# Performance work log

Measured on AMD Instinct MI355X. Metric: run time of the kernel, lower is better.

Reference implementation:

```python
import jax, jax.numpy as jnp
import numpy as np

N = 100000
E = 1600000
IN_C, HID_C, OUT_C = 128, 128, 64


def setup_inputs() -> dict:
    key = jax.random.key(0)
    k = jax.random.split(key, 8)
    x = jax.random.normal(k[0], (N, IN_C), dtype=jnp.float32)
    edge_index = jax.random.randint(k[1], (2, E), 0, N, dtype=jnp.int64)
    edge_attr = jax.random.uniform(k[2], (E,), dtype=jnp.float32)
    # Glorot-ish init for GCNConv weights, zero bias (PyG default)
    W1 = jax.random.normal(k[3], (IN_C, HID_C), dtype=jnp.float32) / np.sqrt(IN_C)
    b1 = jnp.zeros((HID_C,), dtype=jnp.float32)
    W2 = jax.random.normal(k[4], (HID_C, OUT_C), dtype=jnp.float32) / np.sqrt(HID_C)
    b2 = jnp.zeros((OUT_C,), dtype=jnp.float32)
    return {"x": x, "edge_index": edge_index, "edge_attr": edge_attr,
            "W1": W1, "b1": b1, "W2": W2, "b2": b2}


def _gcn_conv(x, W, b, src, dst, ew):
    """PyG GCNConv: add self-loops (weight 1), symmetric normalization,
    aggregate x@W over edges src->dst, add bias."""
    n = x.shape[0]
    loop = jnp.arange(n, dtype=src.dtype)
    src_f = jnp.concatenate([src, loop])            # [E+N]
    dst_f = jnp.concatenate([dst, loop])
    ew_f = jnp.concatenate([ew, jnp.ones((n,), dtype=ew.dtype)])
    deg = jax.ops.segment_sum(ew_f, dst_f, num_segments=n)  # [N]
    dis = jnp.where(deg > 0, jax.lax.rsqrt(jnp.maximum(deg, 1e-12)), 0.0)
    norm = dis[src_f] * ew_f * dis[dst_f]           # [E+N]
    h = x @ W                                       # [N, C_out]
    msg = norm[:, None] * h[src_f]                  # [E+N, C_out] gather
    out = jax.ops.segment_sum(msg, dst_f, num_segments=n)   # scatter-add
    return out + b


def reference(x, edge_index, edge_attr, W1, b1, W2, b2):
    src, dst = edge_index[0], edge_index[1]
    h = _gcn_conv(x, W1, b1, src, dst, edge_attr)
    h = jax.nn.relu(h)
    # dropout is identity in eval mode (training=False)
    out = _gcn_conv(h, W2, b2, src, dst, edge_attr)
    return out
```

## Files before the change

### kernel.cpp

```cpp
#include <hip/hip_runtime.h>

#define NN 100000
#define EE 1600000
#define NB 391

typedef unsigned int uint;
typedef unsigned short ushort;
typedef unsigned long long u64;

#define FIXMASK ((1ull << 40) - 1)

__device__ inline ushort f2bf(float f) {
    uint u = __float_as_uint(f);
    return (ushort)((u + 0x7fffu + ((u >> 16) & 1u)) >> 16);
}
__device__ inline float bf_lo(uint u) { return __uint_as_float(u << 16); }
__device__ inline float bf_hi(uint u) { return __uint_as_float(u & 0xffff0000u); }

__global__ void k_init(u64* __restrict__ dh) {
    int i = blockIdx.x * blockDim.x + threadIdx.x;
    if (i < NN) dh[i] = 0ull;
}

__global__ void k_dh(const int* __restrict__ dst, const float* __restrict__ ew,
                     u64* __restrict__ dh) {
    int e = blockIdx.x * blockDim.x + threadIdx.x;
    if (e >= EE) return;
    int d = dst[e];
    u64 w = (u64)(ew[e] * 16777216.0f + 0.5f);
    atomicAdd(&dh[d], (1ull << 40) | w);
}

__global__ __launch_bounds__(256) void k_scan_blk(const u64* __restrict__ dh,
                                                  float* __restrict__ dis,
                                                  int* __restrict__ rowptr,
                                                  int* __restrict__ bsum) {
    __shared__ int buf[2][256];
    int t = threadIdx.x;
    int i = blockIdx.x * 256 + t;
    int v = 0;
    if (i < NN) {
        u64 p = dh[i];
        v = (int)(p >> 40);
        float deg = 1.0f + (float)(p & FIXMASK) * (1.0f / 16777216.0f);
        dis[i] = rsqrtf(deg);
    }
    int pi = 0;
    buf[0][t] = v;
    __syncthreads();
    for (int off = 1; off < 256; off <<= 1) {
        int po = pi ^ 1;
        int add = (t >= off) ? buf[pi][t - off] : 0;
        buf[po][t] = buf[pi][t] + add;
        __syncthreads();
        pi = po;
    }
    int incl = buf[pi][t];
    if (i < NN) rowptr[i] = incl - v;
    if (t == 255) bsum[blockIdx.x] = incl;
}

__global__ __launch_bounds__(512) void k_scan_top(int* __restrict__ bsum) {
    __shared__ int buf[2][512];
    int t = threadIdx.x;
    int v = (t < NB) ? bsum[t] : 0;
    int pi = 0;
    buf[0][t] = v;
    __syncthreads();
    for (int off = 1; off < 512; off <<= 1) {
        int po = pi ^ 1;
        int add = (t >= off) ? buf[pi][t - off] : 0;
        buf[po][t] = buf[pi][t] + add;
        __syncthreads();
        pi = po;
    }
    int incl = buf[pi][t];
    if (t < NB) bsum[t] = incl - v;
}

__global__ void k_scan_add(int* __restrict__ rowptr, const int* __restrict__ bsum,
                           int* __restrict__ cursor) {
    int i = blockIdx.x * 256 + threadIdx.x;
    if (i < NN) {
        int r = rowptr[i] + bsum[i >> 8];
        rowptr[i] = r;
        cursor[i] = r;
    }
    if (i == 0) rowptr[NN] = EE;
}

__global__ void k_scatter(const int* __restrict__ src, const int* __restrict__ dst,
                          const float* __restrict__ ew, const float* __restrict__ dis,
                          int* __restrict__ cursor, int2* __restrict__ epk) {
    int e = blockIdx.x * blockDim.x + threadIdx.x;
    if (e >= EE) return;
    int d = dst[e];
    int s = src[e];
    int pos = atomicAdd(&cursor[d], 1);
    float w = dis[s] * ew[e];
    epk[pos] = make_int2(s, __float_as_int(w));
}

__global__ __launch_bounds__(256) void k_gemm1(const float* __restrict__ x,
                                               const float* __restrict__ W,
                                               ushort* __restrict__ h) {
    __shared__ float Wl[128 * 128];
    __shared__ float xt[128 * 32];
    int t = threadIdx.x;
    int rb = blockIdx.x * 32;

    const float4* W4 = (const float4*)W;
    float4* Wl4 = (float4*)Wl;
#pragma unroll
    for (int i = 0; i < 16; i++) Wl4[t + 256 * i] = W4[t + 256 * i];

#pragma unroll
    for (int i = 0; i < 4; i++) {
        int idx = t + 256 * i;
        int r = idx >> 5;
        int c4 = idx & 31;
        float4 v = ((const float4*)(x + (size_t)(rb + r) * 128))[c4];
        int kc = c4 << 2;
        xt[(kc + 0) * 32 + r] = v.x;
        xt[(kc + 1) * 32 + r] = v.y;
        xt[(kc + 2) * 32 + r] = v.z;
        xt[(kc + 3) * 32 + r] = v.w;
    }
    __syncthreads();

    int tc = t & 31;
    int tr = t >> 5;
    float acc[4][4] = {};
#pragma unroll 4
    for (int k = 0; k < 128; k++) {
        float4 wv = ((const float4*)(Wl + k * 128))[tc];
        float4 xv = ((const float4*)(xt + k * 32))[tr];
        float xs[4] = {xv.x, xv.y, xv.z, xv.w};
        float ws[4] = {wv.x, wv.y, wv.z, wv.w};
#pragma unroll
        for (int r = 0; r < 4; r++)
#pragma unroll
            for (int c = 0; c < 4; c++) acc[r][c] += xs[r] * ws[c];
    }
#pragma unroll
    for (int r = 0; r < 4; r++) {
        int row = rb + tr * 4 + r;
        ushort4 o = {f2bf(acc[r][0]), f2bf(acc[r][1]), f2bf(acc[r][2]), f2bf(acc[r][3])};
        ((ushort4*)(h + (size_t)row * 128))[tc] = o;
    }
}

__global__ __launch_bounds__(256) void k_gemm2(const float* __restrict__ a,
                                               const float* __restrict__ W,
                                               ushort* __restrict__ h) {
    __shared__ float Wl[128 * 64];
    __shared__ float at[128 * 64];
    int t = threadIdx.x;
    int rb = blockIdx.x * 64;

    const float4* W4 = (const float4*)W;
    float4* Wl4 = (float4*)Wl;
#pragma unroll
    for (int i = 0; i < 8; i++) Wl4[t + 256 * i] = W4[t + 256 * i];

#pragma unroll
    for (int i = 0; i < 8; i++) {
        int idx = t + 256 * i;
        int r = idx >> 5;
        int c4 = idx & 31;
        int row = rb + r;
        if (row >= NN) row = NN - 1;
        float4 v = ((const float4*)(a + (size_t)row * 128))[c4];
        int kc = c4 << 2;
        at[(kc + 0) * 64 + r] = v.x;
        at[(kc + 1) * 64 + r] = v.y;
        at[(kc + 2) * 64 + r] = v.z;
        at[(kc + 3) * 64 + r] = v.w;
    }
    __syncthreads();

    int tc = t & 15;
    int tr = t >> 4;
    float acc[4][4] = {};
#pragma unroll 4
    for (int k = 0; k < 128; k++) {
        float4 wv = ((const float4*)(Wl + k * 64))[tc];
        float4 av = ((const float4*)(at + k * 64))[tr];
        float as[4] = {av.x, av.y, av.z, av.w};
        float ws[4] = {wv.x, wv.y, wv.z, wv.w};
#pragma unroll
        for (int r = 0; r < 4; r++)
#pragma unroll
            for (int c = 0; c < 4; c++) acc[r][c] += as[r] * ws[c];
    }
#pragma unroll
    for (int r = 0; r < 4; r++) {
        int row = rb + tr * 4 + r;
        if (row < NN) {
            ushort4 o = {f2bf(acc[r][0]), f2bf(acc[r][1]), f2bf(acc[r][2]), f2bf(acc[r][3])};
            ((ushort4*)(h + (size_t)row * 64))[tc] = o;
        }
    }
}

__global__ __launch_bounds__(256) void k_agg1(const int* __restrict__ rowptr,
                                              const int2* __restrict__ epk,
                                              const float* __restrict__ dis,
                                              const ushort* __restrict__ h,
                                              const float* __restrict__ b,
                                              float* __restrict__ a) {
    int wid = (blockIdx.x * blockDim.x + threadIdx.x) >> 6;
    int lane = threadIdx.x & 63;
    if (wid >= NN) return;
    int beg = rowptr[wid], end = rowptr[wid + 1];
    const uint* hp = (const uint*)h;
    uint us = hp[(size_t)wid * 64 + lane];
    float di = dis[wid];
    float2 bv = ((const float2*)b)[lane];

    float2 acc0 = {0.f, 0.f}, acc1 = {0.f, 0.f};
    float2 acc2 = {0.f, 0.f}, acc3 = {0.f, 0.f};
    int j = beg;
    for (; j + 3 < end; j += 4) {
        int2 p0 = epk[j];
        int2 p1 = epk[j + 1];
        int2 p2 = epk[j + 2];
        int2 p3 = epk[j + 3];
        uint u0 = hp[(size_t)p0.x * 64 + lane];
        uint u1 = hp[(size_t)p1.x * 64 + lane];
        uint u2 = hp[(size_t)p2.x * 64 + lane];
        uint u3 = hp[(size_t)p3.x * 64 + lane];
        float w0 = __int_as_float(p0.y);
        float w1 = __int_as_float(p1.y);
        float w2 = __int_as_float(p2.y);
        float w3 = __int_as_float(p3.y);
        acc0.x += w0 * bf_lo(u0); acc0.y += w0 * bf_hi(u0);
        acc1.x += w1 * bf_lo(u1); acc1.y += w1 * bf_hi(u1);
        acc2.x += w2 * bf_lo(u2); acc2.y += w2 * bf_hi(u2);
        acc3.x += w3 * bf_lo(u3); acc3.y += w3 * bf_hi(u3);
    }
    for (; j < end; j++) {
        int2 p0 = epk[j];
        float w0 = __int_as_float(p0.y);
        uint u0 = hp[(size_t)p0.x * 64 + lane];
        acc0.x += w0 * bf_lo(u0); acc0.y += w0 * bf_hi(u0);
    }
    float sx = (acc0.x + acc1.x) + (acc2.x + acc3.x);
    float sy = (acc0.y + acc1.y) + (acc2.y + acc3.y);
    float ox = di * sx + di * di * bf_lo(us) + bv.x;
    float oy = di * sy + di * di * bf_hi(us) + bv.y;
    float2 o = {fmaxf(ox, 0.f), fmaxf(oy, 0.f)};
    ((float2*)a)[(size_t)wid * 64 + lane] = o;
}

__global__ __launch_bounds__(256) void k_agg2(const int* __restrict__ rowptr,
                                              const int2* __restrict__ epk,
                                              const float* __restrict__ dis,
                                              const ushort* __restrict__ h,
                                              const float* __restrict__ b,
                                              float* __restrict__ out) {
    int wid = (blockIdx.x * blockDim.x + threadIdx.x) >> 6;
    int lane = threadIdx.x & 63;
    if (wid >= NN) return;
    int beg = rowptr[wid], end = rowptr[wid + 1];
    float hv = __uint_as_float(((uint)h[(size_t)wid * 64 + lane]) << 16);
    float di = dis[wid];
    float bl = b[lane];

    float acc0 = 0.f, acc1 = 0.f, acc2 = 0.f, acc3 = 0.f;
    int j = beg;
    for (; j + 3 < end; j += 4) {
        int2 p0 = epk[j];
        int2 p1 = epk[j + 1];
        int2 p2 = epk[j + 2];
        int2 p3 = epk[j + 3];
        float v0 = __uint_as_float(((uint)h[(size_t)p0.x * 64 + lane]) << 16);
        float v1 = __uint_as_float(((uint)h[(size_t)p1.x * 64 + lane]) << 16);
        float v2 = __uint_as_float(((uint)h[(size_t)p2.x * 64 + lane]) << 16);
        float v3 = __uint_as_float(((uint)h[(size_t)p3.x * 64 + lane]) << 16);
        acc0 += __int_as_float(p0.y) * v0;
        acc1 += __int_as_float(p1.y) * v1;
        acc2 += __int_as_float(p2.y) * v2;
        acc3 += __int_as_float(p3.y) * v3;
    }
    for (; j < end; j++) {
        int2 p0 = epk[j];
        acc0 += __int_as_float(p0.y) *
                __uint_as_float(((uint)h[(size_t)p0.x * 64 + lane]) << 16);
    }
    float s = (acc0 + acc1) + (acc2 + acc3);
    out[(size_t)wid * 64 + lane] = di * s + di * di * hv + bl;
}

extern "C" void kernel_launch(void* const* d_in, const int* in_sizes, int n_in,
                              void* d_out, int out_size, void* d_ws, size_t ws_size,
                              hipStream_t stream) {
    const float* x  = (const float*)d_in[0];
    const int* ei   = (const int*)d_in[1];
    const float* ew = (const float*)d_in[2];
    const float* W1 = (const float*)d_in[3];
    const float* b1 = (const float*)d_in[4];
    const float* W2 = (const float*)d_in[5];
    const float* b2 = (const float*)d_in[6];
    float* out      = (float*)d_out;

    const int* src = ei;
    const int* dst = ei + EE;

    u64* dh     = (u64*)d_ws;
    float* dis  = (float*)(dh + 102400);
    int* rowptr = (int*)(dis + 102400);
    int* cursor = rowptr + 102528;
    int* bsum   = cursor + 102400;
    int2* epk   = (int2*)(bsum + 512);
    ushort* hb  = (ushort*)(epk + EE);
    float* a1   = (float*)(hb + (size_t)NN * 128);

    k_init<<<NB, 256, 0, stream>>>(dh);
    k_dh<<<EE / 256, 256, 0, stream>>>(dst, ew, dh);
    k_scan_blk<<<NB, 256, 0, stream>>>(dh, dis, rowptr, bsum);
    k_scan_top<<<1, 512, 0, stream>>>(bsum);
    k_scan_add<<<NB, 256, 0, stream>>>(rowptr, bsum, cursor);
    k_scatter<<<EE / 256, 256, 0, stream>>>(src, dst, ew, dis, cursor, epk);

    k_gemm1<<<NN / 32, 256, 0, stream>>>(x, W1, hb);
    k_agg1<<<(NN * 64 + 255) / 256, 256, 0, stream>>>(rowptr, epk, dis, hb, b1, a1);

    k_gemm2<<<(NN + 63) / 64, 256, 0, stream>>>(a1, W2, hb);
    k_agg2<<<(NN * 64 + 255) / 256, 256, 0, stream>>>(rowptr, epk, dis, hb, b2, out);
}
```

Before: 538.2 us.

## Build CSR via two-level bucket sort instead of per-edge global atomics

The old CSR build did a global atomic degree histogram, a three-kernel scan, and an atomic-cursor scatter into 100k node counters. It is replaced by a coarse count of destination buckets (256 nodes each), a single-block bucket scan, a binning pass that writes packed 64-bit edge records, and a per-bucket LDS counting sort. The per-bucket sort also computes degrees, `dis` and `rowptr`. Because `dis` is now only known after sorting, the source-side normalisation `dis[src]` moves into both aggregation kernels as an extra gather per edge. `epk` reuses the `recs` buffer in place, which relies on each bucket fitting within the LDS capacity `CAP`; a larger bucket could overwrite records before they are read.

```diff
diff --git a/kernel.cpp b/kernel.cpp
--- a/kernel.cpp
+++ b/kernel.cpp
@@ -2,14 +2,15 @@
 
 #define NN 100000
 #define EE 1600000
-#define NB 391
+#define NBKT 391
+#define NCHK 391
+#define BINCHUNK 4096
+#define CAP 5120
 
 typedef unsigned int uint;
 typedef unsigned short ushort;
 typedef unsigned long long u64;
 
-#define FIXMASK ((1ull << 40) - 1)
-
 __device__ inline ushort f2bf(float f) {
     uint u = __float_as_uint(f);
     return (ushort)((u + 0x7fffu + ((u >> 16) & 1u)) >> 16);
@@ -17,53 +18,27 @@
 __device__ inline float bf_lo(uint u) { return __uint_as_float(u << 16); }
 __device__ inline float bf_hi(uint u) { return __uint_as_float(u & 0xffff0000u); }
 
-__global__ void k_init(u64* __restrict__ dh) {
-    int i = blockIdx.x * blockDim.x + threadIdx.x;
-    if (i < NN) dh[i] = 0ull;
-}
-
-__global__ void k_dh(const int* __restrict__ dst, const float* __restrict__ ew,
-                     u64* __restrict__ dh) {
-    int e = blockIdx.x * blockDim.x + threadIdx.x;
-    if (e >= EE) return;
-    int d = dst[e];
-    u64 w = (u64)(ew[e] * 16777216.0f + 0.5f);
-    atomicAdd(&dh[d], (1ull << 40) | w);
-}
-
-__global__ __launch_bounds__(256) void k_scan_blk(const u64* __restrict__ dh,
-                                                  float* __restrict__ dis,
-                                                  int* __restrict__ rowptr,
-                                                  int* __restrict__ bsum) {
-    __shared__ int buf[2][256];
-    int t = threadIdx.x;
-    int i = blockIdx.x * 256 + t;
-    int v = 0;
-    if (i < NN) {
-        u64 p = dh[i];
-        v = (int)(p >> 40);
-        float deg = 1.0f + (float)(p & FIXMASK) * (1.0f / 16777216.0f);
-        dis[i] = rsqrtf(deg);
-    }
-    int pi = 0;
-    buf[0][t] = v;
-    __syncthreads();
-    for (int off = 1; off < 256; off <<= 1) {
-        int po = pi ^ 1;
-        int add = (t >= off) ? buf[pi][t - off] : 0;
-        buf[po][t] = buf[pi][t] + add;
-        __syncthreads();
-        pi = po;
-    }
-    int incl = buf[pi][t];
-    if (i < NN) rowptr[i] = incl - v;
-    if (t == 255) bsum[blockIdx.x] = incl;
-}
-
-__global__ __launch_bounds__(512) void k_scan_top(int* __restrict__ bsum) {
+__global__ __launch_bounds__(256) void k_count(const int* __restrict__ dst,
+                                               int* __restrict__ gcount) {
+    __shared__ int bh[NBKT];
+    int t = threadIdx.x;
+    for (int i = t; i < NBKT; i += 256) bh[i] = 0;
+    __syncthreads();
+    int base = blockIdx.x * BINCHUNK;
+    int lim = min(EE - base, BINCHUNK);
+    for (int i = t; i < lim; i += 256) atomicAdd(&bh[dst[base + i] >> 8], 1);
+    __syncthreads();
+    for (int i = t; i < NBKT; i += 256)
+        if (bh[i]) atomicAdd(&gcount[i], bh[i]);
+}
+
+__global__ __launch_bounds__(512) void k_bscan(const int* __restrict__ gcount,
+                                               int* __restrict__ bofs,
+                                               int* __restrict__ gcursor,
+                                               int* __restrict__ rowptr) {
     __shared__ int buf[2][512];
     int t = threadIdx.x;
-    int v = (t < NB) ? bsum[t] : 0;
+    int v = (t < NBKT) ? gcount[t] : 0;
     int pi = 0;
     buf[0][t] = v;
     __syncthreads();
@@ -74,31 +49,84 @@
         __syncthreads();
         pi = po;
     }
-    int incl = buf[pi][t];
-    if (t < NB) bsum[t] = incl - v;
-}
-
-__global__ void k_scan_add(int* __restrict__ rowptr, const int* __restrict__ bsum,
-                           int* __restrict__ cursor) {
-    int i = blockIdx.x * 256 + threadIdx.x;
-    if (i < NN) {
-        int r = rowptr[i] + bsum[i >> 8];
-        rowptr[i] = r;
-        cursor[i] = r;
-    }
-    if (i == 0) rowptr[NN] = EE;
-}
-
-__global__ void k_scatter(const int* __restrict__ src, const int* __restrict__ dst,
-                          const float* __restrict__ ew, const float* __restrict__ dis,
-                          int* __restrict__ cursor, int2* __restrict__ epk) {
-    int e = blockIdx.x * blockDim.x + threadIdx.x;
-    if (e >= EE) return;
-    int d = dst[e];
-    int s = src[e];
-    int pos = atomicAdd(&cursor[d], 1);
-    float w = dis[s] * ew[e];
-    epk[pos] = make_int2(s, __float_as_int(w));
+    int excl = buf[pi][t] - v;
+    if (t < NBKT) { bofs[t] = excl; gcursor[t] = excl; }
+    if (t == 0) { bofs[NBKT] = EE; rowptr[NN] = EE; }
+}
+
+__global__ __launch_bounds__(256) void k_bin(const int* __restrict__ src,
+                                             const int* __restrict__ dst,
+                                             const float* __restrict__ ew,
+                                             int* __restrict__ gcursor,
+                                             u64* __restrict__ recs) {
+    __shared__ int bh[NBKT], start[NBKT], lc[NBKT];
+    int t = threadIdx.x;
+    for (int i = t; i < NBKT; i += 256) { bh[i] = 0; lc[i] = 0; }
+    __syncthreads();
+    int base = blockIdx.x * BINCHUNK;
+    int lim = min(EE - base, BINCHUNK);
+    for (int i = t; i < lim; i += 256) atomicAdd(&bh[dst[base + i] >> 8], 1);
+    __syncthreads();
+    for (int i = t; i < NBKT; i += 256)
+        if (bh[i]) start[i] = atomicAdd(&gcursor[i], bh[i]);
+    __syncthreads();
+    for (int i = t; i < lim; i += 256) {
+        int e = base + i;
+        int d = dst[e];
+        int b = d >> 8;
+        int r = atomicAdd(&lc[b], 1);
+        recs[start[b] + r] = ((u64)__float_as_uint(ew[e]) << 25) |
+                             ((u64)(uint)src[e] << 8) | (u64)(uint)(d & 255);
+    }
+}
+
+__global__ __launch_bounds__(256) void k_sort(const u64* __restrict__ recs,
+                                              const int* __restrict__ bofs,
+                                              float* __restrict__ dis,
+                                              int* __restrict__ rowptr,
+                                              int2* __restrict__ epk) {
+    __shared__ u64 rl[CAP];
+    __shared__ int hist[256], cur[256];
+    __shared__ float degf[256];
+    __shared__ int sb[2][256];
+    int t = threadIdx.x;
+    int b = blockIdx.x;
+    int base = bofs[b], cnt = bofs[b + 1] - base;
+    hist[t] = 0; cur[t] = 0; degf[t] = 0.f;
+    __syncthreads();
+    for (int i = t; i < cnt; i += 256) {
+        u64 r = recs[base + i];
+        if (i < CAP) rl[i] = r;
+        int dl = (int)(r & 255);
+        atomicAdd(&hist[dl], 1);
+        atomicAdd(&degf[dl], __uint_as_float((uint)(r >> 25)));
+    }
+    __syncthreads();
+    int v = hist[t];
+    int pi = 0;
+    sb[0][t] = v;
+    __syncthreads();
+    for (int off = 1; off < 256; off <<= 1) {
+        int po = pi ^ 1;
+        int add = (t >= off) ? sb[pi][t - off] : 0;
+        sb[po][t] = sb[pi][t] + add;
+        __syncthreads();
+        pi = po;
+    }
+    int lofs = sb[pi][t] - v;
+    int node = (b << 8) + t;
+    if (node < NN) {
+        dis[node] = rsqrtf(1.0f + degf[t]);
+        rowptr[node] = base + lofs;
+    }
+    hist[t] = lofs;
+    __syncthreads();
+    for (int i = t; i < cnt; i += 256) {
+        u64 r = (i < CAP) ? rl[i] : recs[base + i];
+        int dl = (int)(r & 255);
+        int pos = hist[dl] + atomicAdd(&cur[dl], 1);
+        epk[base + pos] = make_int2((int)((r >> 8) & 0x1FFFF), (int)(uint)(r >> 25));
+    }
 }
 
 __global__ __launch_bounds__(256) void k_gemm1(const float* __restrict__ x,
@@ -230,10 +258,10 @@
         uint u1 = hp[(size_t)p1.x * 64 + lane];
         uint u2 = hp[(size_t)p2.x * 64 + lane];
         uint u3 = hp[(size_t)p3.x * 64 + lane];
-        float w0 = __int_as_float(p0.y);
-        float w1 = __int_as_float(p1.y);
-        float w2 = __int_as_float(p2.y);
-        float w3 = __int_as_float(p3.y);
+        float w0 = dis[p0.x] * __int_as_float(p0.y);
+        float w1 = dis[p1.x] * __int_as_float(p1.y);
+        float w2 = dis[p2.x] * __int_as_float(p2.y);
+        float w3 = dis[p3.x] * __int_as_float(p3.y);
         acc0.x += w0 * bf_lo(u0); acc0.y += w0 * bf_hi(u0);
         acc1.x += w1 * bf_lo(u1); acc1.y += w1 * bf_hi(u1);
         acc2.x += w2 * bf_lo(u2); acc2.y += w2 * bf_hi(u2);
@@ -241,7 +269,7 @@
     }
     for (; j < end; j++) {
         int2 p0 = epk[j];
-        float w0 = __int_as_float(p0.y);
+        float w0 = dis[p0.x] * __int_as_float(p0.y);
         uint u0 = hp[(size_t)p0.x * 64 + lane];
         acc0.x += w0 * bf_lo(u0); acc0.y += w0 * bf_hi(u0);
     }
@@ -278,14 +306,14 @@
         float v1 = __uint_as_float(((uint)h[(size_t)p1.x * 64 + lane]) << 16);
         float v2 = __uint_as_float(((uint)h[(size_t)p2.x * 64 + lane]) << 16);
         float v3 = __uint_as_float(((uint)h[(size_t)p3.x * 64 + lane]) << 16);
-        acc0 += __int_as_float(p0.y) * v0;
-        acc1 += __int_as_float(p1.y) * v1;
-        acc2 += __int_as_float(p2.y) * v2;
-        acc3 += __int_as_float(p3.y) * v3;
+        acc0 += dis[p0.x] * __int_as_float(p0.y) * v0;
+        acc1 += dis[p1.x] * __int_as_float(p1.y) * v1;
+        acc2 += dis[p2.x] * __int_as_float(p2.y) * v2;
+        acc3 += dis[p3.x] * __int_as_float(p3.y) * v3;
     }
     for (; j < end; j++) {
         int2 p0 = epk[j];
-        acc0 += __int_as_float(p0.y) *
+        acc0 += dis[p0.x] * __int_as_float(p0.y) *
                 __uint_as_float(((uint)h[(size_t)p0.x * 64 + lane]) << 16);
     }
     float s = (acc0 + acc1) + (acc2 + acc3);
@@ -307,21 +335,21 @@
     const int* src = ei;
     const int* dst = ei + EE;
 
-    u64* dh     = (u64*)d_ws;
-    float* dis  = (float*)(dh + 102400);
-    int* rowptr = (int*)(dis + 102400);
-    int* cursor = rowptr + 102528;
-    int* bsum   = cursor + 102400;
-    int2* epk   = (int2*)(bsum + 512);
-    ushort* hb  = (ushort*)(epk + EE);
-    float* a1   = (float*)(hb + (size_t)NN * 128);
-
-    k_init<<<NB, 256, 0, stream>>>(dh);
-    k_dh<<<EE / 256, 256, 0, stream>>>(dst, ew, dh);
-    k_scan_blk<<<NB, 256, 0, stream>>>(dh, dis, rowptr, bsum);
-    k_scan_top<<<1, 512, 0, stream>>>(bsum);
-    k_scan_add<<<NB, 256, 0, stream>>>(rowptr, bsum, cursor);
-    k_scatter<<<EE / 256, 256, 0, stream>>>(src, dst, ew, dis, cursor, epk);
+    int* gcount  = (int*)d_ws;
+    int* bofs    = gcount + 512;
+    int* gcursor = bofs + 512;
+    float* dis   = (float*)(gcursor + 512);
+    int* rowptr  = (int*)(dis + 100000);
+    u64* recs    = (u64*)(rowptr + 100002);
+    int2* epk    = (int2*)recs;
+    ushort* hb   = (ushort*)(recs + EE);
+    float* a1    = (float*)(hb + (size_t)NN * 128);
+
+    hipMemsetAsync(gcount, 0, 512 * sizeof(int), stream);
+    k_count<<<NCHK, 256, 0, stream>>>(dst, gcount);
+    k_bscan<<<1, 512, 0, stream>>>(gcount, bofs, gcursor, rowptr);
+    k_bin<<<NCHK, 256, 0, stream>>>(src, dst, ew, gcursor, recs);
+    k_sort<<<NBKT, 256, 0, stream>>>(recs, bofs, dis, rowptr, epk);
 
     k_gemm1<<<NN / 32, 256, 0, stream>>>(x, W1, hb);
     k_agg1<<<(NN * 64 + 255) / 256, 256, 0, stream>>>(rowptr, epk, dis, hb, b1, a1);
```

Result: faster. 467.7 us (-13.1%).
